# Kernel optimization log

Measured on AMD Instinct MI355X. Metric: run time of the kernel, lower is better.

## Reference

```python
import jax, jax.numpy as jnp
import numpy as np

B = 16384
TEXT_D = 768
TECH_D = 256
IN_D = TEXT_D + TECH_D  # 1024
OUT_D = 1024
E = 8


def setup_inputs() -> dict:
    key = jax.random.key(0)
    ks = jax.random.split(key, 8)
    s_in = 1.0 / np.sqrt(IN_D)
    s_out = 1.0 / np.sqrt(OUT_D)
    return {
        "text_features": jax.random.normal(ks[0], (B, TEXT_D), jnp.float32),
        "technical_features": jax.random.normal(ks[1], (B, TECH_D), jnp.float32),
        # stacked expert params: layer1 [E, IN_D, OUT_D], layer2 [E, OUT_D, OUT_D]
        "W1": jax.random.uniform(ks[2], (E, IN_D, OUT_D), jnp.float32, -s_in, s_in),
        "b1": jax.random.uniform(ks[3], (E, OUT_D), jnp.float32, -s_in, s_in),
        "W2": jax.random.uniform(ks[4], (E, OUT_D, OUT_D), jnp.float32, -s_out, s_out),
        "b2": jax.random.uniform(ks[5], (E, OUT_D), jnp.float32, -s_out, s_out),
        # gating network
        "Wg": jax.random.uniform(ks[6], (IN_D, E), jnp.float32, -s_in, s_in),
        "bg": jax.random.uniform(ks[7], (E,), jnp.float32, -s_in, s_in),
    }


def reference(text_features, technical_features, W1, b1, W2, b2, Wg, bg):
    x = jnp.concatenate([text_features, technical_features], axis=-1)  # [B, IN_D]
    gates = jax.nn.softmax(x @ Wg + bg, axis=-1)                       # [B, E]
    h = jax.nn.relu(jnp.einsum('bi,eio->beo', x, W1) + b1[None])       # [B, E, OUT_D]
    y = jnp.einsum('beo,eop->bep', h, W2) + b2[None]                   # [B, E, OUT_D]
    return jnp.einsum('be,bep->bp', gates, y)                          # [B, OUT_D]
```

## Files before the change

### kernel.cpp

```cpp
#include <hip/hip_runtime.h>
#include <hip/hip_bf16.h>

#define NB 16384
#define TEXT_D 768
#define TECH_D 256
#define IND 1024
#define OUTD 1024
#define NE 8
#define KH2 4096

typedef unsigned short u16;
typedef __bf16 bf16x8 __attribute__((ext_vector_type(8)));
typedef float f32x4 __attribute__((ext_vector_type(4)));

__device__ __forceinline__ u16 f2bf(float f) {
  union { float f; unsigned int u; } x; x.f = f;
  unsigned int u = x.u;
  return (u16)((u + 0x7FFFu + ((u >> 16) & 1u)) >> 16);
}

__device__ __forceinline__ void gload_lds16(const void* g, void* l) {
  __builtin_amdgcn_global_load_lds(
      (const __attribute__((address_space(1))) unsigned int*)g,
      (__attribute__((address_space(3))) unsigned int*)l, 16, 0, 0);
}

__global__ __launch_bounds__(256) void convert_gates(
    const float* __restrict__ text, const float* __restrict__ tech,
    const float* __restrict__ Wg, const float* __restrict__ bg,
    u16* __restrict__ xb, float* __restrict__ gates) {
  int t = threadIdx.x;
  int wave = t >> 6, lane = t & 63;
  int row = blockIdx.x * 4 + wave;

  float acc[NE];
#pragma unroll
  for (int e = 0; e < NE; ++e) acc[e] = 0.f;

#pragma unroll
  for (int j = 0; j < 4; ++j) {
    int col = j * 256 + lane * 4;
    float4 v = (j < 3) ? *(const float4*)&text[(size_t)row * TEXT_D + col]
                       : *(const float4*)&tech[(size_t)row * TECH_D + lane * 4];
    ushort4 o = make_ushort4(f2bf(v.x), f2bf(v.y), f2bf(v.z), f2bf(v.w));
    *(ushort4*)&xb[(size_t)row * IND + col] = o;
    const float* wp = &Wg[(size_t)col * NE];
    float xv[4] = {v.x, v.y, v.z, v.w};
#pragma unroll
    for (int i = 0; i < 4; ++i) {
      float4 w0 = *(const float4*)&wp[i * NE];
      float4 w1 = *(const float4*)&wp[i * NE + 4];
      acc[0] = fmaf(xv[i], w0.x, acc[0]);
      acc[1] = fmaf(xv[i], w0.y, acc[1]);
      acc[2] = fmaf(xv[i], w0.z, acc[2]);
      acc[3] = fmaf(xv[i], w0.w, acc[3]);
      acc[4] = fmaf(xv[i], w1.x, acc[4]);
      acc[5] = fmaf(xv[i], w1.y, acc[5]);
      acc[6] = fmaf(xv[i], w1.z, acc[6]);
      acc[7] = fmaf(xv[i], w1.w, acc[7]);
    }
  }
#pragma unroll
  for (int off = 32; off; off >>= 1)
#pragma unroll
    for (int e = 0; e < NE; ++e) acc[e] += __shfl_xor(acc[e], off);

#pragma unroll
  for (int e = 0; e < NE; ++e) acc[e] += bg[e];
  float mx = acc[0];
#pragma unroll
  for (int e = 1; e < NE; ++e) mx = fmaxf(mx, acc[e]);
  float s = 0.f;
#pragma unroll
  for (int e = 0; e < NE; ++e) { acc[e] = expf(acc[e] - mx); s += acc[e]; }
  float inv = 1.f / s;
  if (lane < NE) gates[(size_t)row * NE + lane] = acc[lane] * inv;
}

__global__ __launch_bounds__(256) void transpose_w12(
    const float* __restrict__ W1, const float* __restrict__ W2,
    u16* __restrict__ W1t, u16* __restrict__ W2t) {
  __shared__ u16 tile[64][65];
  int bid = blockIdx.x;
  int half = bid >> 11;
  int b2 = bid & 2047;
  int e = b2 >> 8;
  int tb = b2 & 255;
  int r0 = (tb >> 4) * 64;
  int c0 = (tb & 15) * 64;
  const float* We; u16* Wte; int ostride;
  if (half == 0) {
    We = W1 + (size_t)e * IND * OUTD;
    Wte = W1t + ((size_t)e << 20);
    ostride = 1024;
  } else {
    We = W2 + (size_t)e * IND * OUTD;
    Wte = W2t + ((size_t)(e >> 2) << 22) + (size_t)(e & 3) * 1024;
    ostride = KH2;
  }
  int t = threadIdx.x;
  int tr = t >> 4;
  int s  = t & 15;
  int tc = s * 4;
#pragma unroll
  for (int j = 0; j < 4; ++j) {
    int row = j * 16 + tr;
    float4 v = *(const float4*)&We[(size_t)(r0 + row) * OUTD + c0 + tc];
    tile[row][tc + 0] = f2bf(v.x);
    tile[row][tc + 1] = f2bf(v.y);
    tile[row][tc + 2] = f2bf(v.z);
    tile[row][tc + 3] = f2bf(v.w);
  }
  __syncthreads();
#pragma unroll
  for (int j = 0; j < 4; ++j) {
    int row = j * 16 + tr;
    ushort4 o;
    if (half == 0) {
      o = make_ushort4(tile[tc + 0][row], tile[tc + 1][row],
                       tile[tc + 2][row], tile[tc + 3][row]);
    } else {
      o = make_ushort4(tile[s][row], tile[s + 16][row],
                       tile[s + 32][row], tile[s + 48][row]);
    }
    *(ushort4*)&Wte[(size_t)(c0 + row) * ostride + r0 + tc] = o;
  }
}

#define BAR() asm volatile("s_barrier" ::: "memory")
#define VM0() asm volatile("s_waitcnt vmcnt(0)" ::: "memory")
#define VM2() asm volatile("s_waitcnt vmcnt(2)" ::: "memory")
#define VM6() asm volatile("s_waitcnt vmcnt(6)" ::: "memory")
#define LG0()                                            \
  do {                                                   \
    asm volatile("s_waitcnt lgkmcnt(0)" ::: "memory");   \
    __builtin_amdgcn_sched_barrier(0);                   \
  } while (0)

template <int SLOT, int K>
__device__ __forceinline__ void stage_slot(
    const u16* __restrict__ g, char* buf, int k0,
    int ch0, int rsub, int koff, int lbyte) {
#pragma unroll
  for (int j = 0; j < 2; ++j) {
    int ch = ch0 + j;
    int r;
    if constexpr (SLOT == 0)      r = (ch >> 3) * 128 + (ch & 7) * 8 + rsub;
    else if constexpr (SLOT == 3) r = 64 + (ch >> 3) * 128 + (ch & 7) * 8 + rsub;
    else if constexpr (SLOT == 1) r = (ch >> 2) * 64 + (ch & 3) * 8 + rsub;
    else                          r = (ch >> 2) * 64 + 32 + (ch & 3) * 8 + rsub;
    gload_lds16(g + (size_t)r * K + k0 + koff, buf + r * 128 + lbyte);
  }
}

template <int QH>
__device__ __forceinline__ void load_a(const char* rb, int wr, int lr, int hi,
                                       int swr, bf16x8 (&a)[4][2]) {
#pragma unroll
  for (int i = 0; i < 4; ++i)
#pragma unroll
    for (int ks = 0; ks < 2; ++ks)
      a[i][ks] = *(const bf16x8*)(rb + (wr * 128 + QH * 64 + i * 16 + lr) * 128
                                  + ((ks * 64 + hi * 16) ^ swr));
}

template <int NH>
__device__ __forceinline__ void load_b(const char* rb, int wc, int lr, int hi,
                                       int swr, bf16x8 (&b)[2][2]) {
#pragma unroll
  for (int q = 0; q < 2; ++q)
#pragma unroll
    for (int ks = 0; ks < 2; ++ks)
      b[q][ks] = *(const bf16x8*)(rb +
                                  (wc * 64 + (NH * 2 + q) * 16 + lr) * 128
                                  + ((ks * 64 + hi * 16) ^ swr));
}

template <int MH, int NH>
__device__ __forceinline__ void mfma_quad(const bf16x8 (&a)[4][2],
                                          const bf16x8 (&b)[2][2],
                                          f32x4 (&acc)[8][4]) {
  __builtin_amdgcn_s_setprio(1);
#pragma unroll
  for (int i = 0; i < 4; ++i)
#pragma unroll
    for (int q = 0; q < 2; ++q) {
      acc[MH*4+i][NH*2+q] = __builtin_amdgcn_mfma_f32_16x16x32_bf16(
          a[i][0], b[q][0], acc[MH*4+i][NH*2+q], 0, 0, 0);
      acc[MH*4+i][NH*2+q] = __builtin_amdgcn_mfma_f32_16x16x32_bf16(
          a[i][1], b[q][1], acc[MH*4+i][NH*2+q], 0, 0, 0);
    }
  __builtin_amdgcn_s_setprio(0);
}

template <bool LAST, int K>
__device__ __forceinline__ void tile4(
    const u16* __restrict__ pA, const u16* __restrict__ pB,
    const char* rA, const char* rB, char* sA, char* sB, int kN,
    int ch0, int rsub, int koff, int lbyte,
    int wr, int wc, int lr, int hi, int swr,
    bf16x8 (&a0)[4][2], bf16x8 (&a1)[4][2],
    bf16x8 (&b0)[2][2], bf16x8 (&b1)[2][2],
    f32x4 (&acc)[8][4]) {
  LG0();
  mfma_quad<0, 0>(a0, b0, acc);
  load_b<1>(rB, wc, lr, hi, swr, b1);
  if constexpr (!LAST) {
    stage_slot<0, K>(pA, sA, kN, ch0, rsub, koff, lbyte);
    stage_slot<1, K>(pB, sB, kN, ch0, rsub, koff, lbyte);
    stage_slot<2, K>(pB, sB, kN, ch0, rsub, koff, lbyte);
    VM6();
  } else {
    VM0();
  }
  BAR();
  LG0();
  mfma_quad<0, 1>(a0, b1, acc);
  load_a<1>(rA, wr, lr, hi, swr, a1);
  if constexpr (!LAST)
    stage_slot<3, K>(pA, sA, kN, ch0, rsub, koff, lbyte);
  BAR();
  LG0();
  mfma_quad<1, 0>(a1, b0, acc);
  if constexpr (!LAST) { VM2(); }
  BAR();
  mfma_quad<1, 1>(a1, b1, acc);
  if constexpr (!LAST) {
    load_a<0>(sA, wr, lr, hi, swr, a0);
    load_b<0>(sB, wc, lr, hi, swr, b0);
  }
  BAR();
}

template <int K>
__device__ __forceinline__ void core256(const u16* __restrict__ pA,
                                        const u16* __restrict__ pB,
                                        char* lds, int t, f32x4 (&acc)[8][4]) {
  constexpr int KT = K / 64;
  static_assert(KT >= 2, "KT must be >= 2");
  const int l = t & 63;
  const int w = t >> 6;
  const int wr = w >> 2, wc = w & 3;
  const int lr = l & 15, hi = l >> 4;
  const int rsub = l >> 3;
  const int koff = ((l & 7) ^ rsub) << 3;
  const int lbyte = (l & 7) * 16;
  const int ch0 = w * 2;
  const int swr = (lr & 7) << 4;

  char* A0 = lds;
  char* A1 = lds + 32768;
  char* B0 = lds + 65536;
  char* B1 = lds + 98304;

  bf16x8 a0[4][2], a1[4][2], b0[2][2], b1[2][2];

  stage_slot<0, K>(pA, A0, 0, ch0, rsub, koff, lbyte);
  stage_slot<1, K>(pB, B0, 0, ch0, rsub, koff, lbyte);
  stage_slot<2, K>(pB, B0, 0, ch0, rsub, koff, lbyte);
  stage_slot<3, K>(pA, A0, 0, ch0, rsub, koff, lbyte);
  VM2(); BAR();
  load_a<0>(A0, wr, lr, hi, swr, a0);
  load_b<0>(B0, wc, lr, hi, swr, b0);

  char *rA = A0, *rB = B0, *sA = A1, *sB = B1;
  for (int T = 0; T < KT - 1; ++T) {
    tile4<false, K>(pA, pB, rA, rB, sA, sB, (T + 1) * 64,
                    ch0, rsub, koff, lbyte, wr, wc, lr, hi, swr,
                    a0, a1, b0, b1, acc);
    char* x = rA; rA = sA; sA = x;
    x = rB; rB = sB; sB = x;
  }
  tile4<true, K>(pA, pB, rA, rB, sA, sB, 0,
                 ch0, rsub, koff, lbyte, wr, wc, lr, hi, swr,
                 a0, a1, b0, b1, acc);
}

__global__ __launch_bounds__(512, 2) void gemm1(
    const u16* __restrict__ xb, const u16* __restrict__ W1t,
    const float* __restrict__ b1, const float* __restrict__ gates,
    u16* __restrict__ Hg, int eg0) {
  __shared__ char lds[131072];
  int t = threadIdx.x;
  int nwg = gridDim.x, cpx = nwg >> 3, bid = blockIdx.x;
  int swz = (bid & 7) * cpx + (bid >> 3);
  int nb = swz & 3, ee = (swz >> 2) & 3, mb = swz >> 4;
  int e = eg0 + ee;

  f32x4 acc[8][4] = {};
  core256<1024>(xb + (size_t)mb * 256 * 1024,
                W1t + ((size_t)e << 20) + (size_t)nb * 256 * 1024,
                lds, t, acc);

  int l = t & 63, w = t >> 6, wr = w >> 2, wc = w & 3, lr = l & 15, hi = l >> 4;
  int m0 = mb * 256 + wr * 128 + hi * 4;
  int n0 = nb * 256 + wc * 64 + lr;
  int nst = nb * 256 + wc * 64 + lr * 4;
  const float* b1e = b1 + e * OUTD;
  float bv[4];
#pragma unroll
  for (int nn = 0; nn < 4; ++nn) bv[nn] = b1e[n0 + nn * 16];
#pragma unroll
  for (int m = 0; m < 8; ++m) {
#pragma unroll
    for (int r = 0; r < 4; ++r) {
      int row = m0 + m * 16 + r;
      float g = gates[(size_t)row * NE + e];
      ushort4 o;
      o.x = f2bf(g * fmaxf(acc[m][0][r] + bv[0], 0.f));
      o.y = f2bf(g * fmaxf(acc[m][1][r] + bv[1], 0.f));
      o.z = f2bf(g * fmaxf(acc[m][2][r] + bv[2], 0.f));
      o.w = f2bf(g * fmaxf(acc[m][3][r] + bv[3], 0.f));
      *(ushort4*)&Hg[(size_t)row * KH2 + ee * 1024 + nst] = o;
    }
  }
}

template <bool FIRST>
__global__ __launch_bounds__(512, 2) void gemm2(
    const u16* __restrict__ Hg, const u16* __restrict__ W2th,
    const float* __restrict__ b2h, const float* __restrict__ gates,
    float* __restrict__ out, int eg0) {
  __shared__ char lds[131072];
  int t = threadIdx.x;
  int nwg = gridDim.x, cpx = nwg >> 3, bid = blockIdx.x;
  int swz = (bid & 7) * cpx + (bid >> 3);
  int nb = swz & 3, mb = swz >> 2;

  f32x4 acc[8][4] = {};
  core256<KH2>(Hg + (size_t)mb * 256 * KH2, W2th + (size_t)nb * 256 * KH2,
               lds, t, acc);

  int l = t & 63, w = t >> 6, wr = w >> 2, wc = w & 3, lr = l & 15, hi = l >> 4;
  int m0 = mb * 256 + wr * 128 + hi * 4;
  int n0 = nb * 256 + wc * 64 + lr;

  float bcol[4][4];
#pragma unroll
  for (int nn = 0; nn < 4; ++nn)
#pragma unroll
    for (int j = 0; j < 4; ++j)
      bcol[nn][j] = b2h[j * OUTD + n0 + nn * 16];

#pragma unroll
  for (int m = 0; m < 8; ++m) {
#pragma unroll
    for (int r = 0; r < 4; ++r) {
      int row = m0 + m * 16 + r;
      float4 ga = *(const float4*)&gates[(size_t)row * NE + eg0];
#pragma unroll
      for (int nn = 0; nn < 4; ++nn) {
        float bias = ga.x * bcol[nn][0] + ga.y * bcol[nn][1] +
                     ga.z * bcol[nn][2] + ga.w * bcol[nn][3];
        size_t oi = (size_t)row * OUTD + n0 + nn * 16;
        float v = acc[m][nn][r] + bias;
        if (FIRST) out[oi] = v;
        else       out[oi] += v;
      }
    }
  }
}

extern "C" void kernel_launch(void* const* d_in, const int* in_sizes, int n_in,
                              void* d_out, int out_size, void* d_ws, size_t ws_size,
                              hipStream_t stream) {
  (void)in_sizes; (void)n_in; (void)out_size; (void)ws_size;
  const float* text = (const float*)d_in[0];
  const float* tech = (const float*)d_in[1];
  const float* W1   = (const float*)d_in[2];
  const float* b1   = (const float*)d_in[3];
  const float* W2   = (const float*)d_in[4];
  const float* b2   = (const float*)d_in[5];
  const float* Wg   = (const float*)d_in[6];
  const float* bg   = (const float*)d_in[7];
  float* out = (float*)d_out;

  char* p = (char*)d_ws;
  u16* xb  = (u16*)p;  p += (size_t)NB * IND * 2;
  u16* W1t = (u16*)p;  p += (size_t)NE * IND * OUTD * 2;
  u16* W2t = (u16*)p;  p += (size_t)NE * OUTD * OUTD * 2;
  float* gates = (float*)p; p += (size_t)NB * NE * 4;
  u16* Hg  = (u16*)p;

  convert_gates<<<dim3(NB / 4), dim3(256), 0, stream>>>(text, tech, Wg, bg, xb, gates);
  transpose_w12<<<dim3(4096), dim3(256), 0, stream>>>(W1, W2, W1t, W2t);

  for (int h = 0; h < 2; ++h) {
    int eg0 = h * 4;
    gemm1<<<dim3(1024), dim3(512), 0, stream>>>(xb, W1t, b1, gates, Hg, eg0);
    const u16* W2th = W2t + ((size_t)h << 22);
    const float* b2h = b2 + (size_t)eg0 * OUTD;
    if (h == 0)
      gemm2<true><<<dim3(256), dim3(512), 0, stream>>>(Hg, W2th, b2h, gates, out, eg0);
    else
      gemm2<false><<<dim3(256), dim3(512), 0, stream>>>(Hg, W2th, b2h, gates, out, eg0);
  }
}
```

Measured before the change: 572.0 us.

## Restructure GEMM main loop to prefetch two K-tiles ahead with fewer barriers

The 256x256 bf16 MFMA core loop moves from a four-phase tile with four barriers per K-step to a two-barrier schedule. Global-to-LDS staging now runs two tiles ahead instead of one, writing into the buffer just consumed. LDS fragment reads for the next tile are interleaved with the MFMA quads, and the sched_barrier is separated from the lgkmcnt wait. The goal is less barrier and wait stall time and more latency hiding. In exchange, the in-place restaging and the wait counts become harder to get right.

```diff
diff --git a/kernel.cpp b/kernel.cpp
--- a/kernel.cpp
+++ b/kernel.cpp
@@ -131,11 +131,9 @@
 #define VM0() asm volatile("s_waitcnt vmcnt(0)" ::: "memory")
 #define VM2() asm volatile("s_waitcnt vmcnt(2)" ::: "memory")
 #define VM6() asm volatile("s_waitcnt vmcnt(6)" ::: "memory")
-#define LG0()                                            \
-  do {                                                   \
-    asm volatile("s_waitcnt lgkmcnt(0)" ::: "memory");   \
-    __builtin_amdgcn_sched_barrier(0);                   \
-  } while (0)
+#define VM8() asm volatile("s_waitcnt vmcnt(8)" ::: "memory")
+#define LGD() asm volatile("s_waitcnt lgkmcnt(0)" ::: "memory")
+#define SB()  __builtin_amdgcn_sched_barrier(0)
 
 template <int SLOT, int K>
 __device__ __forceinline__ void stage_slot(
@@ -193,42 +191,41 @@
   __builtin_amdgcn_s_setprio(0);
 }
 
-template <bool LAST, int K>
-__device__ __forceinline__ void tile4(
+template <int MODE, int K>
+__device__ __forceinline__ void tile2(
     const u16* __restrict__ pA, const u16* __restrict__ pB,
-    const char* rA, const char* rB, char* sA, char* sB, int kN,
+    char* Acur, char* Bcur, const char* Anxt, const char* Bnxt, int k2,
     int ch0, int rsub, int koff, int lbyte,
     int wr, int wc, int lr, int hi, int swr,
     bf16x8 (&a0)[4][2], bf16x8 (&a1)[4][2],
     bf16x8 (&b0)[2][2], bf16x8 (&b1)[2][2],
     f32x4 (&acc)[8][4]) {
-  LG0();
+  if constexpr (MODE == 0) {
+    stage_slot<0, K>(pA, Acur, k2, ch0, rsub, koff, lbyte);
+    stage_slot<1, K>(pB, Bcur, k2, ch0, rsub, koff, lbyte);
+    stage_slot<2, K>(pB, Bcur, k2, ch0, rsub, koff, lbyte);
+  }
+  load_a<1>(Acur, wr, lr, hi, swr, a1);
+  SB();
   mfma_quad<0, 0>(a0, b0, acc);
-  load_b<1>(rB, wc, lr, hi, swr, b1);
-  if constexpr (!LAST) {
-    stage_slot<0, K>(pA, sA, kN, ch0, rsub, koff, lbyte);
-    stage_slot<1, K>(pB, sB, kN, ch0, rsub, koff, lbyte);
-    stage_slot<2, K>(pB, sB, kN, ch0, rsub, koff, lbyte);
-    VM6();
-  } else {
-    VM0();
-  }
+  mfma_quad<0, 1>(a0, b1, acc);
+  LGD();
+  if constexpr (MODE == 0) { VM6(); }
+  else if constexpr (MODE == 1) { VM0(); }
   BAR();
-  LG0();
-  mfma_quad<0, 1>(a0, b1, acc);
-  load_a<1>(rA, wr, lr, hi, swr, a1);
-  if constexpr (!LAST)
-    stage_slot<3, K>(pA, sA, kN, ch0, rsub, koff, lbyte);
-  BAR();
-  LG0();
+  if constexpr (MODE == 0)
+    stage_slot<3, K>(pA, Acur, k2, ch0, rsub, koff, lbyte);
+  if constexpr (MODE < 2)
+    load_a<0>(Anxt, wr, lr, hi, swr, a0);
+  SB();
   mfma_quad<1, 0>(a1, b0, acc);
-  if constexpr (!LAST) { VM2(); }
-  BAR();
+  if constexpr (MODE < 2)
+    load_b<0>(Bnxt, wc, lr, hi, swr, b0);
   mfma_quad<1, 1>(a1, b1, acc);
-  if constexpr (!LAST) {
-    load_a<0>(sA, wr, lr, hi, swr, a0);
-    load_b<0>(sB, wc, lr, hi, swr, b0);
-  }
+  if constexpr (MODE < 2)
+    load_b<1>(Bnxt, wc, lr, hi, swr, b1);
+  LGD();
+  if constexpr (MODE == 0) { VM2(); }
   BAR();
 }
 
@@ -237,7 +234,7 @@
                                         const u16* __restrict__ pB,
                                         char* lds, int t, f32x4 (&acc)[8][4]) {
   constexpr int KT = K / 64;
-  static_assert(KT >= 2, "KT must be >= 2");
+  static_assert(KT >= 4, "KT must be >= 4");
   const int l = t & 63;
   const int w = t >> 6;
   const int wr = w >> 2, wc = w & 3;
@@ -259,21 +256,46 @@
   stage_slot<1, K>(pB, B0, 0, ch0, rsub, koff, lbyte);
   stage_slot<2, K>(pB, B0, 0, ch0, rsub, koff, lbyte);
   stage_slot<3, K>(pA, A0, 0, ch0, rsub, koff, lbyte);
-  VM2(); BAR();
+  stage_slot<0, K>(pA, A1, 64, ch0, rsub, koff, lbyte);
+  stage_slot<1, K>(pB, B1, 64, ch0, rsub, koff, lbyte);
+  stage_slot<2, K>(pB, B1, 64, ch0, rsub, koff, lbyte);
+  stage_slot<3, K>(pA, A1, 64, ch0, rsub, koff, lbyte);
+  VM8(); BAR();
   load_a<0>(A0, wr, lr, hi, swr, a0);
   load_b<0>(B0, wc, lr, hi, swr, b0);
-
-  char *rA = A0, *rB = B0, *sA = A1, *sB = B1;
-  for (int T = 0; T < KT - 1; ++T) {
-    tile4<false, K>(pA, pB, rA, rB, sA, sB, (T + 1) * 64,
-                    ch0, rsub, koff, lbyte, wr, wc, lr, hi, swr,
-                    a0, a1, b0, b1, acc);
-    char* x = rA; rA = sA; sA = x;
-    x = rB; rB = sB; sB = x;
-  }
-  tile4<true, K>(pA, pB, rA, rB, sA, sB, 0,
-                 ch0, rsub, koff, lbyte, wr, wc, lr, hi, swr,
-                 a0, a1, b0, b1, acc);
+  load_b<1>(B0, wc, lr, hi, swr, b1);
+  LGD(); BAR();
+
+  for (int T = 0; T < KT - 2; ++T) {
+    char* Acur = (T & 1) ? A1 : A0;
+    char* Bcur = (T & 1) ? B1 : B0;
+    char* Anxt = (T & 1) ? A0 : A1;
+    char* Bnxt = (T & 1) ? B0 : B1;
+    tile2<0, K>(pA, pB, Acur, Bcur, Anxt, Bnxt, (T + 2) * 64,
+                ch0, rsub, koff, lbyte, wr, wc, lr, hi, swr,
+                a0, a1, b0, b1, acc);
+  }
+  {
+    constexpr int T = 0;
+  }
+  {
+    int T = KT - 2;
+    char* Acur = (T & 1) ? A1 : A0;
+    char* Bcur = (T & 1) ? B1 : B0;
+    char* Anxt = (T & 1) ? A0 : A1;
+    char* Bnxt = (T & 1) ? B0 : B1;
+    tile2<1, K>(pA, pB, Acur, Bcur, Anxt, Bnxt, 0,
+                ch0, rsub, koff, lbyte, wr, wc, lr, hi, swr,
+                a0, a1, b0, b1, acc);
+    T = KT - 1;
+    Acur = (T & 1) ? A1 : A0;
+    Bcur = (T & 1) ? B1 : B0;
+    Anxt = (T & 1) ? A0 : A1;
+    Bnxt = (T & 1) ? B0 : B1;
+    tile2<2, K>(pA, pB, Acur, Bcur, Anxt, Bnxt, 0,
+                ch0, rsub, koff, lbyte, wr, wc, lr, hi, swr,
+                a0, a1, b0, b1, acc);
+  }
 }
 
 __global__ __launch_bounds__(512, 2) void gemm1(
```

Measured after the change: 581.1 us. No clear change (+1.6%).
